# Kernel tuning notes

Hardware: AMD Instinct MI355X
Metric: run time of the kernel (lower is better)

Reference implementation:

```python
import jax, jax.numpy as jnp
import numpy as np
import math

B, T, D, H, K = 4, 2048, 1024, 16, 64

def setup_inputs() -> dict:
    key = jax.random.key(0)
    ks = jax.random.split(key, 6)
    scale = 1.0 / math.sqrt(D)  # keep logits in a sane range (torch code uses raw randn params)
    X = jax.random.normal(ks[0], (B, T, D), dtype=jnp.float32)
    Wq = jax.random.normal(ks[1], (H, D, K), dtype=jnp.float32) * scale
    Wk = jax.random.normal(ks[2], (H, D, K), dtype=jnp.float32) * scale
    Wv = jax.random.normal(ks[3], (H, D, K), dtype=jnp.float32) * scale
    Wo = jax.random.normal(ks[4], (H * K, H * K), dtype=jnp.float32) * (1.0 / math.sqrt(H * K))
    bo = jnp.zeros((H * K,), dtype=jnp.float32)
    return {"X": X, "Wq": Wq, "Wk": Wk, "Wv": Wv, "Wo": Wo, "bo": bo}

def reference(X, Wq, Wk, Wv, Wo, bo):
    # per-head projections: [B,H,T,K]
    q = jnp.einsum('btc,nck->bntk', X, Wq)
    k = jnp.einsum('btc,nck->bntk', X, Wk)
    v = jnp.einsum('btc,nck->bntk', X, Wv)
    # full score matrix [B,H,T,T] with causal mask (query t attends to s <= t)
    scores = jnp.einsum('bntk,bnsk->bnts', q, k) / math.sqrt(K)
    causal = jnp.tril(jnp.ones((T, T), dtype=bool))
    scores = jnp.where(causal[None, None], scores, jnp.finfo(scores.dtype).min)
    attn = jax.nn.softmax(scores, axis=-1)
    out = jnp.einsum('bnts,bnsk->bntk', attn, v)  # [B,H,T,K]
    # concat heads along feature dim (head-major ordering, matches torch.cat over heads)
    out = jnp.transpose(out, (0, 2, 1, 3)).reshape(B, T, H * K)
    # output projection (torch nn.Linear: x @ W.T + b)
    return out @ Wo.T + bo
```

## Files before the change

### kernel.cpp

```cpp
#include <hip/hip_runtime.h>
#include <hip/hip_bf16.h>
#include <math.h>

#define B_SZ 4
#define T_SZ 2048
#define D_SZ 1024
#define H_SZ 16
#define K_SZ 64

typedef __attribute__((ext_vector_type(8))) short bf8_t;
typedef __attribute__((ext_vector_type(4))) float f4_t;

__device__ __forceinline__ ushort f2bf(float f) {
    union { float f; unsigned u; } v; v.f = f;
    return (ushort)((v.u + 0x7fffu + ((v.u >> 16) & 1u)) >> 16);
}

__device__ __forceinline__ void gld_lds16(const ushort* g, ushort* l) {
    __builtin_amdgcn_global_load_lds(
        (const __attribute__((address_space(1))) void*)g,
        (__attribute__((address_space(3))) void*)l, 16, 0, 0);
}

__global__ __launch_bounds__(256) void convert_bf16_kernel(
    const float* __restrict__ src, ushort* __restrict__ dst)
{
    const size_t i = ((size_t)blockIdx.x * 256 + threadIdx.x) * 8;
    float4 a = *(const float4*)(src + i);
    float4 b = *(const float4*)(src + i + 4);
    ushort o[8] = {f2bf(a.x), f2bf(a.y), f2bf(a.z), f2bf(a.w),
                   f2bf(b.x), f2bf(b.y), f2bf(b.z), f2bf(b.w)};
    *(uint4*)(dst + i) = *(const uint4*)o;
}

__global__ __launch_bounds__(256) void transpose_w_kernel(
    const float* __restrict__ Wq, const float* __restrict__ Wk,
    const float* __restrict__ Wv, ushort* __restrict__ WT)
{
    __shared__ __align__(16) float tile[64][68];
    const int tid = threadIdx.x;
    const int d0  = blockIdx.x * 64;
    const int g   = blockIdx.y;
    const int sel = g >> 4, h = g & 15;
    const float* W = (sel == 0 ? Wq : (sel == 1 ? Wk : Wv)) + (size_t)h * D_SZ * K_SZ;

    {
        const int r = tid >> 2, ks = (tid & 3) * 16;
        const float4* src = (const float4*)(W + (size_t)(d0 + r) * 64 + ks);
        float4* dst = (float4*)&tile[r][ks];
        dst[0] = src[0]; dst[1] = src[1]; dst[2] = src[2]; dst[3] = src[3];
    }
    __syncthreads();
    {
        const int k = tid >> 2, ds = (tid & 3) * 16;
        ushort o[16];
        #pragma unroll
        for (int i = 0; i < 16; ++i) o[i] = f2bf(tile[ds + i][k]);
        uint4* dst = (uint4*)&WT[(size_t)(sel * 1024 + h * 64 + k) * 1024 + d0 + ds];
        dst[0] = ((const uint4*)o)[0];
        dst[1] = ((const uint4*)o)[1];
    }
}

__device__ __forceinline__ void gemm_bt_tile(
    const ushort* __restrict__ A, const ushort* __restrict__ Bt,
    int Kdim, int m0, int n0, ushort* As, ushort* Bs, f4_t acc[4][4])
{
    const int tid  = threadIdx.x;
    const int lane = tid & 63, wv = tid >> 6;
    const int l16  = lane & 15, quad = lane >> 4;
    const int wm   = (wv >> 1) * 64, wn = (wv & 1) * 64;
    const int sw   = (l16 >> 1) & 3;

    const int ra0 = tid >> 2,         qa0 = (tid & 3) ^ ((ra0 >> 1) & 3);
    const int ra1 = (tid + 256) >> 2, qa1 = (tid & 3) ^ ((ra1 >> 1) & 3);
    ushort* ldsA0 = As + (size_t)(wv * 64) * 8;
    ushort* ldsA1 = As + (size_t)(wv * 64 + 256) * 8;
    ushort* ldsB0 = Bs + (size_t)(wv * 64) * 8;
    ushort* ldsB1 = Bs + (size_t)(wv * 64 + 256) * 8;
    const ushort* gA0 = A  + (size_t)(m0 + ra0) * Kdim + qa0 * 8;
    const ushort* gA1 = A  + (size_t)(m0 + ra1) * Kdim + qa1 * 8;
    const ushort* gB0 = Bt + (size_t)(n0 + ra0) * Kdim + qa0 * 8;
    const ushort* gB1 = Bt + (size_t)(n0 + ra1) * Kdim + qa1 * 8;

    for (int k0 = 0; k0 < Kdim; k0 += 32) {
        __syncthreads();
        gld_lds16(gA0 + k0, ldsA0);
        gld_lds16(gA1 + k0, ldsA1);
        gld_lds16(gB0 + k0, ldsB0);
        gld_lds16(gB1 + k0, ldsB1);
        __syncthreads();

        bf8_t a[4], b[4];
        #pragma unroll
        for (int mt = 0; mt < 4; ++mt)
            a[mt] = *(const bf8_t*)&As[(wm + mt * 16 + l16) * 32 + ((quad ^ sw) * 8)];
        #pragma unroll
        for (int nt = 0; nt < 4; ++nt)
            b[nt] = *(const bf8_t*)&Bs[(wn + nt * 16 + l16) * 32 + ((quad ^ sw) * 8)];
        #pragma unroll
        for (int mt = 0; mt < 4; ++mt)
            #pragma unroll
            for (int nt = 0; nt < 4; ++nt)
                acc[mt][nt] = __builtin_amdgcn_mfma_f32_16x16x32_bf16(
                    a[mt], b[nt], acc[mt][nt], 0, 0, 0);
    }
}

__global__ __launch_bounds__(256) void gemm_qkv_kernel(
    const ushort* __restrict__ Xb, const ushort* __restrict__ WT,
    ushort* __restrict__ Qo, ushort* __restrict__ Ko, ushort* __restrict__ Vo)
{
    __shared__ __align__(16) ushort As[128 * 32];
    __shared__ __align__(16) ushort Bs[128 * 32];
    const int n0 = blockIdx.x * 128, m0 = blockIdx.y * 128;

    f4_t acc[4][4];
    #pragma unroll
    for (int i = 0; i < 4; ++i)
        #pragma unroll
        for (int j = 0; j < 4; ++j) acc[i][j] = (f4_t){0.f, 0.f, 0.f, 0.f};

    gemm_bt_tile(Xb, WT, 1024, m0, n0, As, Bs, acc);

    const int tid = threadIdx.x;
    const int lane = tid & 63, wv = tid >> 6;
    const int l16 = lane & 15, quad = lane >> 4;
    const int wm = (wv >> 1) * 64, wn = (wv & 1) * 64;
    const int sel = n0 >> 10;
    ushort* Out = (sel == 0 ? Qo : (sel == 1 ? Ko : Vo));
    const float osc = (sel == 0) ? 0.125f : 1.0f;

    #pragma unroll
    for (int nt = 0; nt < 4; ++nt) {
        const int col = n0 + wn + nt * 16 + l16;
        const int h = (col >> 6) & 15, kk = col & 63;
        #pragma unroll
        for (int mt = 0; mt < 4; ++mt) {
            #pragma unroll
            for (int r = 0; r < 4; ++r) {
                const int row = m0 + wm + mt * 16 + quad * 4 + r;
                const int bb = row >> 11, t = row & 2047;
                Out[((size_t)(bb * 16 + h) * 2048 + t) * 64 + kk] =
                    f2bf(acc[mt][nt][r] * osc);
            }
        }
    }
}

__global__ __launch_bounds__(256) void gemm_out_kernel(
    const ushort* __restrict__ Yb, const ushort* __restrict__ WoB,
    const float* __restrict__ bo, float* __restrict__ Out)
{
    __shared__ __align__(16) ushort As[128 * 32];
    __shared__ __align__(16) ushort Bs[128 * 32];
    const int n0 = blockIdx.x * 128, m0 = blockIdx.y * 128;

    f4_t acc[4][4];
    #pragma unroll
    for (int i = 0; i < 4; ++i)
        #pragma unroll
        for (int j = 0; j < 4; ++j) acc[i][j] = (f4_t){0.f, 0.f, 0.f, 0.f};

    gemm_bt_tile(Yb, WoB, 1024, m0, n0, As, Bs, acc);

    const int tid = threadIdx.x;
    const int lane = tid & 63, wv = tid >> 6;
    const int l16 = lane & 15, quad = lane >> 4;
    const int wm = (wv >> 1) * 64, wn = (wv & 1) * 64;

    #pragma unroll
    for (int nt = 0; nt < 4; ++nt) {
        const int col = n0 + wn + nt * 16 + l16;
        const float bias = bo[col];
        #pragma unroll
        for (int mt = 0; mt < 4; ++mt) {
            #pragma unroll
            for (int r = 0; r < 4; ++r) {
                const int row = m0 + wm + mt * 16 + quad * 4 + r;
                Out[(size_t)row * 1024 + col] = acc[mt][nt][r] + bias;
            }
        }
    }
}

__global__ __launch_bounds__(256) void transpose_v_kernel(
    const ushort* __restrict__ V, ushort* __restrict__ Vt)
{
    __shared__ __align__(16) ushort tile[64 * 74];
    const int tid = threadIdx.x;
    const int t0  = blockIdx.x * 64;
    const int bh  = blockIdx.y;

    {
        const int t = tid >> 2, ks = (tid & 3) * 16;
        const ushort* src = V + ((size_t)bh * T_SZ + t0 + t) * K_SZ + ks;
        uint4 a = *(const uint4*)src;
        uint4 b = *(const uint4*)(src + 8);
        uint* dst = (uint*)&tile[t * 74 + ks];
        dst[0] = a.x; dst[1] = a.y; dst[2] = a.z; dst[3] = a.w;
        dst[4] = b.x; dst[5] = b.y; dst[6] = b.z; dst[7] = b.w;
    }
    __syncthreads();
    {
        const int l = tid & 63, w = tid >> 6;
        #pragma unroll
        for (int kk = 0; kk < 16; ++kk) {
            const int k = w * 16 + kk;
            Vt[((size_t)bh * K_SZ + k) * T_SZ + t0 + l] = tile[l * 74 + k];
        }
    }
}

__global__ __launch_bounds__(256) void attn_mfma_kernel(
    const ushort* __restrict__ Qg, const ushort* __restrict__ Kg,
    const ushort* __restrict__ Vtg, ushort* __restrict__ Y)
{
    __shared__ __align__(16) ushort Ks[2][64 * 64];
    __shared__ __align__(16) ushort Vs[2][64 * 64];
    __shared__ __align__(16) ushort Pl[4][32 * 72];

    const int tid  = threadIdx.x;
    const int w    = tid >> 6;
    const int lane = tid & 63;
    const int l16  = lane & 15;
    const int quad = lane >> 4;
    const int qi = 15 - blockIdx.x;
    const int bh = blockIdx.y;
    const int bb = bh >> 4, h = bh & 15;

    const int Q0   = qi * 128;
    const int trow = Q0 + w * 32;

    bf8_t qa[2][2];
    #pragma unroll
    for (int mt = 0; mt < 2; ++mt) {
        const ushort* qp = Qg + ((size_t)bh * T_SZ + trow + mt * 16 + l16) * K_SZ + quad * 8;
        qa[mt][0] = *(const bf8_t*)qp;
        qa[mt][1] = *(const bf8_t*)(qp + 32);
    }

    f4_t O[2][4];
    #pragma unroll
    for (int mt = 0; mt < 2; ++mt)
        #pragma unroll
        for (int dt = 0; dt < 4; ++dt) O[mt][dt] = (f4_t){0.f, 0.f, 0.f, 0.f};
    float lp[2][4];
    #pragma unroll
    for (int mt = 0; mt < 2; ++mt)
        #pragma unroll
        for (int r = 0; r < 4; ++r) lp[mt][r] = 0.f;

    ushort* myP = Pl[w];
    const int sw_r = ((l16 >> 2) & 3) << 4;
    const int g_ln = (lane & 7) ^ (lane >> 3);
    const int rr_ln = lane >> 3;

    const ushort* Kbh = Kg  + (size_t)bh * T_SZ * K_SZ;
    const ushort* Vbh = Vtg + (size_t)bh * K_SZ * T_SZ;

    const int n_it = 2 * qi + 2;

    #pragma unroll
    for (int j = 0; j < 2; ++j) {
        const int r8 = (j * 4 + w) * 8 + rr_ln;
        gld_lds16(Kbh + (size_t)r8 * K_SZ + g_ln * 8, &Ks[0][(j * 4 + w) * 512]);
        gld_lds16(Vbh + (size_t)r8 * T_SZ + g_ln * 8, &Vs[0][(j * 4 + w) * 512]);
    }

    int cur = 0;
    for (int it = 0; it < n_it; ++it) {
        const int s0 = it * 64;

        __syncthreads();
        if (it + 1 < n_it) {
            const int sn = s0 + 64, nb = cur ^ 1;
            #pragma unroll
            for (int j = 0; j < 2; ++j) {
                const int r8 = (j * 4 + w) * 8 + rr_ln;
                gld_lds16(Kbh + (size_t)(sn + r8) * K_SZ + g_ln * 8,
                          &Ks[nb][(j * 4 + w) * 512]);
                gld_lds16(Vbh + (size_t)r8 * T_SZ + sn + g_ln * 8,
                          &Vs[nb][(j * 4 + w) * 512]);
            }
        }

        if (s0 < trow + 32) {
            const ushort* Kc = Ks[cur];
            const ushort* Vc = Vs[cur];

            bf8_t kb[4][2], vb[4][2];
            #pragma unroll
            for (int nt = 0; nt < 4; ++nt) {
                const int sr = nt * 16 + l16;
                kb[nt][0] = *(const bf8_t*)&Kc[sr * 64 + ((quad ^ (sr & 7)) * 8)];
                kb[nt][1] = *(const bf8_t*)&Kc[sr * 64 + (((quad + 4) ^ (sr & 7)) * 8)];
                vb[nt][0] = *(const bf8_t*)&Vc[sr * 64 + ((quad ^ (sr & 7)) * 8)];
                vb[nt][1] = *(const bf8_t*)&Vc[sr * 64 + (((quad + 4) ^ (sr & 7)) * 8)];
            }

            f4_t S[2][4];
            #pragma unroll
            for (int mt = 0; mt < 2; ++mt)
                #pragma unroll
                for (int nt = 0; nt < 4; ++nt) S[mt][nt] = (f4_t){0.f, 0.f, 0.f, 0.f};
            #pragma unroll
            for (int mt = 0; mt < 2; ++mt)
                #pragma unroll
                for (int nt = 0; nt < 4; ++nt) {
                    S[mt][nt] = __builtin_amdgcn_mfma_f32_16x16x32_bf16(
                        qa[mt][0], kb[nt][0], S[mt][nt], 0, 0, 0);
                    S[mt][nt] = __builtin_amdgcn_mfma_f32_16x16x32_bf16(
                        qa[mt][1], kb[nt][1], S[mt][nt], 0, 0, 0);
                }

            const bool diag = (s0 + 64 > trow);

            #pragma unroll
            for (int mt = 0; mt < 2; ++mt) {
                float p[4][4];
                #pragma unroll
                for (int nt = 0; nt < 4; ++nt) {
                    const int sg = s0 + nt * 16 + l16;
                    #pragma unroll
                    for (int r = 0; r < 4; ++r) {
                        float x = S[mt][nt][r];
                        if (diag && sg > trow + mt * 16 + quad * 4 + r) x = -1e30f;
                        p[nt][r] = __expf(x);
                        lp[mt][r] += p[nt][r];
                    }
                }
                #pragma unroll
                for (int nt = 0; nt < 4; ++nt) {
                    const int colp = (nt * 16 + l16) ^ (quad << 4);
                    #pragma unroll
                    for (int r = 0; r < 4; ++r)
                        myP[(mt * 16 + quad * 4 + r) * 72 + colp] = f2bf(p[nt][r]);
                }
            }
            asm volatile("" ::: "memory");
            bf8_t pa[2][2];
            #pragma unroll
            for (int mt = 0; mt < 2; ++mt) {
                const ushort* pr = &myP[(mt * 16 + l16) * 72];
                pa[mt][0] = *(const bf8_t*)(pr + ((quad * 8) ^ sw_r));
                pa[mt][1] = *(const bf8_t*)(pr + ((32 + quad * 8) ^ sw_r));
            }

            #pragma unroll
            for (int dt = 0; dt < 4; ++dt)
                #pragma unroll
                for (int mt = 0; mt < 2; ++mt) {
                    O[mt][dt] = __builtin_amdgcn_mfma_f32_16x16x32_bf16(
                        pa[mt][0], vb[dt][0], O[mt][dt], 0, 0, 0);
                    O[mt][dt] = __builtin_amdgcn_mfma_f32_16x16x32_bf16(
                        pa[mt][1], vb[dt][1], O[mt][dt], 0, 0, 0);
                }
        }
        cur ^= 1;
    }

    #pragma unroll
    for (int mt = 0; mt < 2; ++mt) {
        float inv[4];
        #pragma unroll
        for (int r = 0; r < 4; ++r) {
            float s = lp[mt][r];
            #pragma unroll
            for (int off = 1; off < 16; off <<= 1)
                s += __shfl_xor(s, off);
            inv[r] = 1.f / s;
        }
        #pragma unroll
        for (int dt = 0; dt < 4; ++dt) {
            const int col = h * 64 + dt * 16 + l16;
            #pragma unroll
            for (int r = 0; r < 4; ++r) {
                const int tg = trow + mt * 16 + quad * 4 + r;
                Y[((size_t)(bb * T_SZ + tg)) * (H_SZ * K_SZ) + col] =
                    f2bf(O[mt][dt][r] * inv[r]);
            }
        }
    }
}

extern "C" void kernel_launch(void* const* d_in, const int* in_sizes, int n_in,
                              void* d_out, int out_size, void* d_ws, size_t ws_size,
                              hipStream_t stream) {
    const float* X  = (const float*)d_in[0];
    const float* Wq = (const float*)d_in[1];
    const float* Wk = (const float*)d_in[2];
    const float* Wv = (const float*)d_in[3];
    const float* Wo = (const float*)d_in[4];
    const float* bo = (const float*)d_in[5];
    float* out = (float*)d_out;

    const size_t NE = (size_t)B_SZ * H_SZ * T_SZ * K_SZ;
    ushort* Qb   = (ushort*)d_ws;
    ushort* Kb   = Qb + NE;
    ushort* Vb   = Kb + NE;
    ushort* Vtb  = Vb + NE;
    ushort* Yb   = Vtb + NE;
    ushort* Xb   = Yb + NE;
    ushort* WT   = Xb + NE;
    ushort* WoB  = WT + (size_t)3072 * 1024;

    convert_bf16_kernel<<<dim3(4096), 256, 0, stream>>>(X, Xb);
    convert_bf16_kernel<<<dim3(512), 256, 0, stream>>>(Wo, WoB);
    transpose_w_kernel<<<dim3(16, 48), 256, 0, stream>>>(Wq, Wk, Wv, WT);
    gemm_qkv_kernel<<<dim3(24, 64), 256, 0, stream>>>(Xb, WT, Qb, Kb, Vb);
    transpose_v_kernel<<<dim3(32, 64), 256, 0, stream>>>(Vb, Vtb);
    attn_mfma_kernel<<<dim3(16, 64), 256, 0, stream>>>(Qb, Kb, Vtb, Yb);
    gemm_out_kernel<<<dim3(8, 64), 256, 0, stream>>>(Yb, WoB, bo, out);
}
```

Before: 340.0 us.

## Pair causal query tiles per block and use exp2 with prescaled Q

Each attention block now handles two query tiles, a low one and its mirrored high one, so every block does the same amount of causal work and each K/V tile loaded into LDS serves both. The grid shrinks to half as many blocks. Q is prescaled by log2(e)/sqrt(K) so the softmax can use the hardware exp2 directly, and the mask compare is skipped on off-diagonal tiles. The cost is doubled accumulator registers, which may lower occupancy, and fewer blocks in flight.

```diff
diff --git a/kernel.cpp b/kernel.cpp
--- a/kernel.cpp
+++ b/kernel.cpp
@@ -21,6 +21,8 @@
         (const __attribute__((address_space(1))) void*)g,
         (__attribute__((address_space(3))) void*)l, 16, 0, 0);
 }
+
+#define Q_PRESCALE 0.18033688011112042f
 
 __global__ __launch_bounds__(256) void convert_bf16_kernel(
     const float* __restrict__ src, ushort* __restrict__ dst)
@@ -129,7 +131,7 @@
     const int wm = (wv >> 1) * 64, wn = (wv & 1) * 64;
     const int sel = n0 >> 10;
     ushort* Out = (sel == 0 ? Qo : (sel == 1 ? Ko : Vo));
-    const float osc = (sel == 0) ? 0.125f : 1.0f;
+    const float osc = (sel == 0) ? Q_PRESCALE : 1.0f;
 
     #pragma unroll
     for (int nt = 0; nt < 4; ++nt) {
@@ -225,31 +227,37 @@
     const int lane = tid & 63;
     const int l16  = lane & 15;
     const int quad = lane >> 4;
-    const int qi = 15 - blockIdx.x;
+    const int qlo = blockIdx.x;
+    const int qhi = 15 - qlo;
     const int bh = blockIdx.y;
     const int bb = bh >> 4, h = bh & 15;
 
-    const int Q0   = qi * 128;
-    const int trow = Q0 + w * 32;
-
-    bf8_t qa[2][2];
+    const int trowL = qlo * 128 + w * 32;
+    const int trowH = qhi * 128 + w * 32;
+
+    bf8_t qaL[2][2], qaH[2][2];
     #pragma unroll
     for (int mt = 0; mt < 2; ++mt) {
-        const ushort* qp = Qg + ((size_t)bh * T_SZ + trow + mt * 16 + l16) * K_SZ + quad * 8;
-        qa[mt][0] = *(const bf8_t*)qp;
-        qa[mt][1] = *(const bf8_t*)(qp + 32);
-    }
-
-    f4_t O[2][4];
-    #pragma unroll
-    for (int mt = 0; mt < 2; ++mt)
-        #pragma unroll
-        for (int dt = 0; dt < 4; ++dt) O[mt][dt] = (f4_t){0.f, 0.f, 0.f, 0.f};
-    float lp[2][4];
-    #pragma unroll
-    for (int mt = 0; mt < 2; ++mt)
-        #pragma unroll
-        for (int r = 0; r < 4; ++r) lp[mt][r] = 0.f;
+        const ushort* qpL = Qg + ((size_t)bh * T_SZ + trowL + mt * 16 + l16) * K_SZ + quad * 8;
+        const ushort* qpH = Qg + ((size_t)bh * T_SZ + trowH + mt * 16 + l16) * K_SZ + quad * 8;
+        qaL[mt][0] = *(const bf8_t*)qpL;
+        qaL[mt][1] = *(const bf8_t*)(qpL + 32);
+        qaH[mt][0] = *(const bf8_t*)qpH;
+        qaH[mt][1] = *(const bf8_t*)(qpH + 32);
+    }
+
+    f4_t OL[2][4], OH[2][4];
+    float lpL[2][4], lpH[2][4];
+    #pragma unroll
+    for (int mt = 0; mt < 2; ++mt) {
+        #pragma unroll
+        for (int dt = 0; dt < 4; ++dt) {
+            OL[mt][dt] = (f4_t){0.f, 0.f, 0.f, 0.f};
+            OH[mt][dt] = (f4_t){0.f, 0.f, 0.f, 0.f};
+        }
+        #pragma unroll
+        for (int r = 0; r < 4; ++r) { lpL[mt][r] = 0.f; lpH[mt][r] = 0.f; }
+    }
 
     ushort* myP = Pl[w];
     const int sw_r = ((l16 >> 2) & 3) << 4;
@@ -259,7 +267,81 @@
     const ushort* Kbh = Kg  + (size_t)bh * T_SZ * K_SZ;
     const ushort* Vbh = Vtg + (size_t)bh * K_SZ * T_SZ;
 
-    const int n_it = 2 * qi + 2;
+    const int n_it = 2 * qhi + 2;
+
+    bf8_t kb[4][2], vb[4][2];
+    int s0 = 0;
+    auto tile_compute = [&](const bf8_t (&qa)[2][2], f4_t (&O)[2][4],
+                            float (&lp)[2][4], int trow) {
+        f4_t S[2][4];
+        #pragma unroll
+        for (int mt = 0; mt < 2; ++mt)
+            #pragma unroll
+            for (int nt = 0; nt < 4; ++nt) S[mt][nt] = (f4_t){0.f, 0.f, 0.f, 0.f};
+        #pragma unroll
+        for (int mt = 0; mt < 2; ++mt)
+            #pragma unroll
+            for (int nt = 0; nt < 4; ++nt) {
+                S[mt][nt] = __builtin_amdgcn_mfma_f32_16x16x32_bf16(
+                    qa[mt][0], kb[nt][0], S[mt][nt], 0, 0, 0);
+                S[mt][nt] = __builtin_amdgcn_mfma_f32_16x16x32_bf16(
+                    qa[mt][1], kb[nt][1], S[mt][nt], 0, 0, 0);
+            }
+
+        const bool diag = (s0 + 64 > trow);
+
+        #pragma unroll
+        for (int mt = 0; mt < 2; ++mt) {
+            float p[4][4];
+            if (diag) {
+                #pragma unroll
+                for (int nt = 0; nt < 4; ++nt) {
+                    const int sg = s0 + nt * 16 + l16;
+                    #pragma unroll
+                    for (int r = 0; r < 4; ++r) {
+                        float x = S[mt][nt][r];
+                        if (sg > trow + mt * 16 + quad * 4 + r) x = -1e30f;
+                        p[nt][r] = __builtin_amdgcn_exp2f(x);
+                        lp[mt][r] += p[nt][r];
+                    }
+                }
+            } else {
+                #pragma unroll
+                for (int nt = 0; nt < 4; ++nt)
+                    #pragma unroll
+                    for (int r = 0; r < 4; ++r) {
+                        p[nt][r] = __builtin_amdgcn_exp2f(S[mt][nt][r]);
+                        lp[mt][r] += p[nt][r];
+                    }
+            }
+            #pragma unroll
+            for (int nt = 0; nt < 4; ++nt) {
+                const int colp = (nt * 16 + l16) ^ (quad << 4);
+                #pragma unroll
+                for (int r = 0; r < 4; ++r)
+                    myP[(mt * 16 + quad * 4 + r) * 72 + colp] = f2bf(p[nt][r]);
+            }
+        }
+        asm volatile("" ::: "memory");
+        bf8_t pa[2][2];
+        #pragma unroll
+        for (int mt = 0; mt < 2; ++mt) {
+            const ushort* pr = &myP[(mt * 16 + l16) * 72];
+            pa[mt][0] = *(const bf8_t*)(pr + ((quad * 8) ^ sw_r));
+            pa[mt][1] = *(const bf8_t*)(pr + ((32 + quad * 8) ^ sw_r));
+        }
+        asm volatile("" ::: "memory");
+
+        #pragma unroll
+        for (int dt = 0; dt < 4; ++dt)
+            #pragma unroll
+            for (int mt = 0; mt < 2; ++mt) {
+                O[mt][dt] = __builtin_amdgcn_mfma_f32_16x16x32_bf16(
+                    pa[mt][0], vb[dt][0], O[mt][dt], 0, 0, 0);
+                O[mt][dt] = __builtin_amdgcn_mfma_f32_16x16x32_bf16(
+                    pa[mt][1], vb[dt][1], O[mt][dt], 0, 0, 0);
+            }
+    };
 
     #pragma unroll
     for (int j = 0; j < 2; ++j) {
@@ -270,7 +352,7 @@
 
     int cur = 0;
     for (int it = 0; it < n_it; ++it) {
-        const int s0 = it * 64;
+        s0 = it * 64;
 
         __syncthreads();
         if (it + 1 < n_it) {
@@ -285,11 +367,11 @@
             }
         }
 
-        if (s0 < trow + 32) {
+        const bool doH = (s0 < trowH + 32);
+        const bool doL = (s0 < trowL + 32);
+        if (doH || doL) {
             const ushort* Kc = Ks[cur];
             const ushort* Vc = Vs[cur];
-
-            bf8_t kb[4][2], vb[4][2];
             #pragma unroll
             for (int nt = 0; nt < 4; ++nt) {
                 const int sr = nt * 16 + l16;
@@ -298,90 +380,38 @@
                 vb[nt][0] = *(const bf8_t*)&Vc[sr * 64 + ((quad ^ (sr & 7)) * 8)];
                 vb[nt][1] = *(const bf8_t*)&Vc[sr * 64 + (((quad + 4) ^ (sr & 7)) * 8)];
             }
-
-            f4_t S[2][4];
-            #pragma unroll
-            for (int mt = 0; mt < 2; ++mt)
+            if (doH) tile_compute(qaH, OH, lpH, trowH);
+            if (doL) tile_compute(qaL, OL, lpL, trowL);
+        }
+        cur ^= 1;
+    }
+
+    auto epilogue = [&](f4_t (&O)[2][4], float (&lp)[2][4], int trow) {
+        #pragma unroll
+        for (int mt = 0; mt < 2; ++mt) {
+            float inv[4];
+            #pragma unroll
+            for (int r = 0; r < 4; ++r) {
+                float s = lp[mt][r];
                 #pragma unroll
-                for (int nt = 0; nt < 4; ++nt) S[mt][nt] = (f4_t){0.f, 0.f, 0.f, 0.f};
-            #pragma unroll
-            for (int mt = 0; mt < 2; ++mt)
+                for (int off = 1; off < 16; off <<= 1)
+                    s += __shfl_xor(s, off);
+                inv[r] = 1.f / s;
+            }
+            #pragma unroll
+            for (int dt = 0; dt < 4; ++dt) {
+                const int col = h * 64 + dt * 16 + l16;
                 #pragma unroll
-                for (int nt = 0; nt < 4; ++nt) {
-                    S[mt][nt] = __builtin_amdgcn_mfma_f32_16x16x32_bf16(
-                        qa[mt][0], kb[nt][0], S[mt][nt], 0, 0, 0);
-                    S[mt][nt] = __builtin_amdgcn_mfma_f32_16x16x32_bf16(
-                        qa[mt][1], kb[nt][1], S[mt][nt], 0, 0, 0);
+                for (int r = 0; r < 4; ++r) {
+                    const int tg = trow + mt * 16 + quad * 4 + r;
+                    Y[((size_t)(bb * T_SZ + tg)) * (H_SZ * K_SZ) + col] =
+                        f2bf(O[mt][dt][r] * inv[r]);
                 }
-
-            const bool diag = (s0 + 64 > trow);
-
-            #pragma unroll
-            for (int mt = 0; mt < 2; ++mt) {
-                float p[4][4];
-                #pragma unroll
-                for (int nt = 0; nt < 4; ++nt) {
-                    const int sg = s0 + nt * 16 + l16;
-                    #pragma unroll
-                    for (int r = 0; r < 4; ++r) {
-                        float x = S[mt][nt][r];
-                        if (diag && sg > trow + mt * 16 + quad * 4 + r) x = -1e30f;
-                        p[nt][r] = __expf(x);
-                        lp[mt][r] += p[nt][r];
-                    }
-                }
-                #pragma unroll
-                for (int nt = 0; nt < 4; ++nt) {
-                    const int colp = (nt * 16 + l16) ^ (quad << 4);
-                    #pragma unroll
-                    for (int r = 0; r < 4; ++r)
-                        myP[(mt * 16 + quad * 4 + r) * 72 + colp] = f2bf(p[nt][r]);
-                }
-            }
-            asm volatile("" ::: "memory");
-            bf8_t pa[2][2];
-            #pragma unroll
-            for (int mt = 0; mt < 2; ++mt) {
-                const ushort* pr = &myP[(mt * 16 + l16) * 72];
-                pa[mt][0] = *(const bf8_t*)(pr + ((quad * 8) ^ sw_r));
-                pa[mt][1] = *(const bf8_t*)(pr + ((32 + quad * 8) ^ sw_r));
-            }
-
-            #pragma unroll
-            for (int dt = 0; dt < 4; ++dt)
-                #pragma unroll
-                for (int mt = 0; mt < 2; ++mt) {
-                    O[mt][dt] = __builtin_amdgcn_mfma_f32_16x16x32_bf16(
-                        pa[mt][0], vb[dt][0], O[mt][dt], 0, 0, 0);
-                    O[mt][dt] = __builtin_amdgcn_mfma_f32_16x16x32_bf16(
-                        pa[mt][1], vb[dt][1], O[mt][dt], 0, 0, 0);
-                }
-        }
-        cur ^= 1;
-    }
-
-    #pragma unroll
-    for (int mt = 0; mt < 2; ++mt) {
-        float inv[4];
-        #pragma unroll
-        for (int r = 0; r < 4; ++r) {
-            float s = lp[mt][r];
-            #pragma unroll
-            for (int off = 1; off < 16; off <<= 1)
-                s += __shfl_xor(s, off);
-            inv[r] = 1.f / s;
-        }
-        #pragma unroll
-        for (int dt = 0; dt < 4; ++dt) {
-            const int col = h * 64 + dt * 16 + l16;
-            #pragma unroll
-            for (int r = 0; r < 4; ++r) {
-                const int tg = trow + mt * 16 + quad * 4 + r;
-                Y[((size_t)(bb * T_SZ + tg)) * (H_SZ * K_SZ) + col] =
-                    f2bf(O[mt][dt][r] * inv[r]);
-            }
-        }
-    }
+            }
+        }
+    };
+    epilogue(OH, lpH, trowH);
+    epilogue(OL, lpL, trowL);
 }
 
 extern "C" void kernel_launch(void* const* d_in, const int* in_sizes, int n_in,
@@ -410,6 +440,6 @@
     transpose_w_kernel<<<dim3(16, 48), 256, 0, stream>>>(Wq, Wk, Wv, WT);
     gemm_qkv_kernel<<<dim3(24, 64), 256, 0, stream>>>(Xb, WT, Qb, Kb, Vb);
     transpose_v_kernel<<<dim3(32, 64), 256, 0, stream>>>(Vb, Vtb);
-    attn_mfma_kernel<<<dim3(16, 64), 256, 0, stream>>>(Qb, Kb, Vtb, Yb);
+    attn_mfma_kernel<<<dim3(8, 64), 256, 0, stream>>>(Qb, Kb, Vtb, Yb);
     gemm_out_kernel<<<dim3(8, 64), 256, 0, stream>>>(Yb, WoB, bo, out);
 }
```

After: 306.9 us. -9.7%, faster.
